# Kernel optimization log

Measured on AMD Instinct MI355X. Metric: run time of the kernel, lower is better.

Reference implementation:

```python
import jax, jax.numpy as jnp
import numpy as np

WS = 8   # window_size
SS = 4   # shift_size
NH = 6   # num_heads
EPS = 1e-5


def _win_partition(x, ws):
    # x: [B, H, W, C] -> [B * H/ws * W/ws, ws*ws, C]
    B, H, W, C = x.shape
    x = x.reshape(B, H // ws, ws, W // ws, ws, C)
    return x.transpose(0, 1, 3, 2, 4, 5).reshape(-1, ws * ws, C)


def _win_reverse(wins, ws, H, W, B):
    C = wins.shape[-1]
    x = wins.reshape(B, H // ws, W // ws, ws, ws, C)
    return x.transpose(0, 1, 3, 2, 4, 5).reshape(B, H, W, C)


def _rel_pos_index(ws):
    # static numpy computation, identical to the torch buffer
    coords = np.stack(np.meshgrid(np.arange(ws), np.arange(ws), indexing='ij')).reshape(2, -1)
    rel = coords[:, :, None] - coords[:, None, :]          # [2, N, N]
    rel = rel.transpose(1, 2, 0).copy()                    # [N, N, 2]
    rel[..., 0] += ws - 1
    rel[..., 1] += ws - 1
    rel[..., 0] *= 2 * ws - 1
    return rel.sum(-1)                                     # [N, N] int


def _attn_mask_np(H, W, ws, ss):
    # static numpy computation of the SW-MSA mask, identical to _compute_mask
    img = np.zeros((1, H, W, 1), np.float32)
    cnt = 0
    for hs in (slice(0, -ws), slice(-ws, -ss), slice(-ss, None)):
        for wsl in (slice(0, -ws), slice(-ws, -ss), slice(-ss, None)):
            img[:, hs, wsl, :] = cnt
            cnt += 1
    mw = img.reshape(1, H // ws, ws, W // ws, ws, 1).transpose(0, 1, 3, 2, 4, 5).reshape(-1, ws * ws)
    am = mw[:, None, :] - mw[:, :, None]                   # [nW, N, N]
    return np.where(am != 0, np.float32(-100.0), np.float32(0.0))


def _swin_forward(x, qkv_w, qkv_b, proj_w, proj_b, rpb_table,
                  norm2_g, norm2_b, mlp_w1, mlp_b1, mlp_w2, mlp_b2, H, W):
    B, L, C = x.shape
    ws, ss, nh = WS, SS, NH
    hd = C // nh
    x2d = x.reshape(B, H, W, C)
    shifted = jnp.roll(x2d, (-ss, -ss), axis=(1, 2))
    win = _win_partition(shifted, ws)                      # [B_, N, C]
    B_, N, _ = win.shape

    # --- window attention (note: original applies attention to un-normalized x) ---
    qkv = (win @ qkv_w + qkv_b).reshape(B_, N, 3, nh, hd)
    q = qkv[:, :, 0].transpose(0, 2, 1, 3)                 # [B_, nh, N, hd]
    k = qkv[:, :, 1].transpose(0, 2, 1, 3)
    v = qkv[:, :, 2].transpose(0, 2, 1, 3)
    attn = jnp.einsum('bhnd,bhmd->bhnm', q, k) * (hd ** -0.5)

    bias = rpb_table[jnp.asarray(_rel_pos_index(ws)).reshape(-1)]
    bias = bias.reshape(N, N, nh).transpose(2, 0, 1)       # [nh, N, N]
    attn = attn + bias[None]

    mask = jnp.asarray(_attn_mask_np(H, W, ws, ss))        # [nW, N, N]
    nW = mask.shape[0]
    attn = attn.reshape(B_ // nW, nW, nh, N, N) + mask[None, :, None]
    attn = jax.nn.softmax(attn.reshape(B_, nh, N, N), axis=-1)

    out = jnp.einsum('bhnm,bhmd->bnhd', attn, v).reshape(B_, N, C)
    out = out @ proj_w + proj_b

    x2d = _win_reverse(out, ws, H, W, B)
    x2d = jnp.roll(x2d, (ss, ss), axis=(1, 2))
    x = x + x2d.reshape(B, L, C)

    # --- MLP branch with LayerNorm (norm2) ---
    mu = x.mean(-1, keepdims=True)
    var = x.var(-1, keepdims=True)
    xn = (x - mu) * jax.lax.rsqrt(var + EPS) * norm2_g + norm2_b
    h = jax.nn.gelu(xn @ mlp_w1 + mlp_b1, approximate=False)
    return x + (h @ mlp_w2 + mlp_b2)


def setup_inputs() -> dict:
    B, H, W, C = 8, 128, 128, 192
    mlp_hidden = 4 * C
    ks = jax.random.split(jax.random.key(0), 6)
    std = 0.02
    return {
        'x': jax.random.normal(ks[0], (B, H * W, C), jnp.float32),
        'qkv_w': jax.random.normal(ks[1], (C, 3 * C), jnp.float32) * std,
        'qkv_b': jnp.zeros((3 * C,), jnp.float32),
        'proj_w': jax.random.normal(ks[2], (C, C), jnp.float32) * std,
        'proj_b': jnp.zeros((C,), jnp.float32),
        'rpb_table': jax.random.normal(ks[3], ((2 * WS - 1) ** 2, NH), jnp.float32) * std,
        'norm2_g': jnp.ones((C,), jnp.float32),
        'norm2_b': jnp.zeros((C,), jnp.float32),
        'mlp_w1': jax.random.normal(ks[4], (C, mlp_hidden), jnp.float32) * std,
        'mlp_b1': jnp.zeros((mlp_hidden,), jnp.float32),
        'mlp_w2': jax.random.normal(ks[5], (mlp_hidden, C), jnp.float32) * std,
        'mlp_b2': jnp.zeros((C,), jnp.float32),
        'H': H,
        'W': W,
    }


def reference(x, qkv_w, qkv_b, proj_w, proj_b, rpb_table, norm2_g, norm2_b,
              mlp_w1, mlp_b1, mlp_w2, mlp_b2, H, W):
    return _swin_forward(x, qkv_w, qkv_b, proj_w, proj_b, rpb_table,
                         norm2_g, norm2_b, mlp_w1, mlp_b1, mlp_w2, mlp_b2, H, W)
```

## Files before the change

kernel.cpp:

```cpp
#include <hip/hip_runtime.h>
#include <hip/hip_bf16.h>


typedef __hip_bfloat16 bf16;
typedef __attribute__((ext_vector_type(8))) short bfrag;
typedef __attribute__((ext_vector_type(4))) float ffrag;

__device__ __forceinline__ float b2f(bf16 v) { return __bfloat162float(v); }
__device__ __forceinline__ bf16  f2b(float v) { return __float2bfloat16(v); }

#define MFMA(a, b, c) __builtin_amdgcn_mfma_f32_16x16x32_bf16((a), (b), (c), 0, 0, 0)

#define WS_XRES  0ULL
#define WS_QKVT  100663296ULL
#define WS_PROJT (WS_QKVT  + 230400ULL)
#define WS_W1T   (WS_PROJT + 76800ULL)
#define WS_W2T   (WS_W1T   + 307200ULL)
#define WS_SB    (WS_W2T   + 331776ULL)

__device__ __forceinline__ float gelu_t(float x) {
    float y = x * (1.5957691216057308f + 0.07135481627f * x * x);
    return x * (1.f / (1.f + __expf(-y)));
}

__global__ __launch_bounds__(256) void k_prep(
    const float* __restrict__ qkv_w, const float* __restrict__ proj_w,
    const float* __restrict__ w1, const float* __restrict__ w2,
    const float* __restrict__ rpb, char* __restrict__ ws)
{
    int i = blockIdx.x * 256 + threadIdx.x;
    bf16* qkvT  = (bf16*)(ws + WS_QKVT);
    bf16* projT = (bf16*)(ws + WS_PROJT);
    bf16* w1T   = (bf16*)(ws + WS_W1T);
    bf16* w2T   = (bf16*)(ws + WS_W2T);
    bf16* sbB   = (bf16*)(ws + WS_SB);

    if (i < 115200) {
        int c = i / 200, k = i % 200;
        qkvT[i] = f2b(k < 192 ? qkv_w[k * 576 + c] : 0.f);
    } else if (i < 153600) {
        int j = i - 115200;
        int c = j / 200, k = j % 200;
        projT[j] = f2b(k < 192 ? proj_w[k * 192 + c] : 0.f);
    } else if (i < 307200) {
        int j = i - 153600;
        int c = j / 200, k = j % 200;
        w1T[j] = f2b(k < 192 ? w1[k * 768 + c] : 0.f);
    } else if (i < 473088) {
        int j = i - 307200;
        int kc = j / 13824, r = (j % 13824) / 72, kk = j % 72;
        w2T[j] = f2b(kk < 64 ? w2[(kc * 64 + kk) * 192 + r] : 0.f);
    } else {
        int j = i - 473088;
        int cls = j / 24576, h = (j % 24576) / 4096;
        int ii = (j % 4096) / 64, jj = j % 64;
        int ri = ii >> 3, ci = ii & 7, rj = jj >> 3, cj = jj & 7;
        float bias = rpb[(((ri - rj + 7) * 15) + (ci - cj + 7)) * 6 + h];
        int clsR = cls >> 1, clsC = cls & 1;
        int regi = (clsR ? (ri < 4 ? 1 : 2) : 0) * 3 + (clsC ? (ci < 4 ? 1 : 2) : 0);
        int regj = (clsR ? (rj < 4 ? 1 : 2) : 0) * 3 + (clsC ? (cj < 4 ? 1 : 2) : 0);
        sbB[j] = f2b(bias + (regi == regj ? 0.f : -100.f));
    }
}

__global__ __launch_bounds__(256, 2) void k_attn(
    const float* __restrict__ x, const float* __restrict__ qkv_b,
    const float* __restrict__ proj_b, const char* __restrict__ ws,
    float* __restrict__ xres)
{
    __shared__ __align__(16) unsigned char smem[75264];
    bf16* sXO = (bf16*)(smem);
    bf16* sQ  = (bf16*)(smem + 25600);
    bf16* sK  = (bf16*)(smem + 38912);
    bf16* sVT = (bf16*)(smem + 52224);
    bf16* sP  = (bf16*)(smem + 66048);

    const bf16* qkvT  = (const bf16*)(ws + WS_QKVT);
    const bf16* projT = (const bf16*)(ws + WS_PROJT);
    const bf16* sbB   = (const bf16*)(ws + WS_SB);

    const int t    = threadIdx.x;
    const int lane = t & 63, quad = lane >> 4, l15 = lane & 15;
    const int wave = t >> 6, r0 = wave * 16;
    const int win = blockIdx.x;
    const int b   = win >> 8;
    const int wi  = win & 255;
    const int wh  = wi >> 4, wwi = wi & 15;

    {
        int row = t >> 2;
        int cg  = (t & 3) * 48;
        int r = row >> 3, c = row & 7;
        int hs  = (wh * 8 + r + 4) & 127;
        int wsX = (wwi * 8 + c + 4) & 127;
        const float4* src = (const float4*)(x + ((size_t)(b * 16384 + hs * 128 + wsX)) * 192 + cg);
        __hip_bfloat162* dst = (__hip_bfloat162*)&sXO[row * 200 + cg];
        #pragma unroll
        for (int u = 0; u < 12; u++) {
            float4 f = src[u];
            dst[u * 2]     = __float22bfloat162_rn({f.x, f.y});
            dst[u * 2 + 1] = __float22bfloat162_rn({f.z, f.w});
        }
    }
    __syncthreads();

    bfrag aX[6];
    #pragma unroll
    for (int kb = 0; kb < 6; kb++)
        aX[kb] = *(const bfrag*)&sXO[(r0 + l15) * 200 + kb * 32 + quad * 8];

    const int cls = ((wh == 15) ? 2 : 0) + ((wwi == 15) ? 1 : 0);
    const bf16* bBc = sbB + (size_t)cls * 24576;

    bf16* sPw = sP + wave * 16 * 72;

    for (int g = 0; g < 2; g++) {
        if (g) __syncthreads();
        #pragma unroll
        for (int part = 0; part < 3; part++) {
            #pragma unroll
            for (int ct = 0; ct < 6; ct++) {
                int col = part * 192 + g * 96 + ct * 16 + l15;
                bfrag bw[6];
                #pragma unroll
                for (int kb = 0; kb < 6; kb++)
                    bw[kb] = *(const bfrag*)&qkvT[col * 200 + kb * 32 + quad * 8];
                ffrag acc = {0.f, 0.f, 0.f, 0.f};
                #pragma unroll
                for (int kb = 0; kb < 6; kb++) acc = MFMA(aX[kb], bw[kb], acc);
                float bias = qkv_b[col];
                #pragma unroll
                for (int reg = 0; reg < 4; reg++) {
                    int r = r0 + quad * 4 + reg;
                    float v = acc[reg] + bias;
                    if (part == 0)      sQ[r * 104 + ct * 16 + l15] = f2b(v);
                    else if (part == 1) sK[r * 104 + ct * 16 + l15] = f2b(v);
                    else {
                        int c96 = ct * 16 + l15;
                        sVT[((c96 >> 5) * 32 + (c96 & 31)) * 72 + r] = f2b(v);
                    }
                }
            }
        }
        __syncthreads();
        for (int hl = 0; hl < 3; hl++) {
            int h = g * 3 + hl;
            bfrag aQ = *(const bfrag*)&sQ[(r0 + l15) * 104 + hl * 32 + quad * 8];
            ffrag Sf[4];
            #pragma unroll
            for (int jt = 0; jt < 4; jt++) {
                bfrag bK = *(const bfrag*)&sK[(jt * 16 + l15) * 104 + hl * 32 + quad * 8];
                ffrag z = {0.f, 0.f, 0.f, 0.f};
                Sf[jt] = MFMA(aQ, bK, z);
            }
            const bf16* bb = bBc + h * 4096 + (r0 + quad * 4) * 64 + l15;
            #pragma unroll
            for (int jt = 0; jt < 4; jt++)
                #pragma unroll
                for (int reg = 0; reg < 4; reg++)
                    Sf[jt][reg] = Sf[jt][reg] * 0.1767766952966369f
                                + b2f(bb[reg * 64 + jt * 16]);
            #pragma unroll
            for (int reg = 0; reg < 4; reg++) {
                float m = fmaxf(fmaxf(Sf[0][reg], Sf[1][reg]), fmaxf(Sf[2][reg], Sf[3][reg]));
                m = fmaxf(m, __shfl_xor(m, 1)); m = fmaxf(m, __shfl_xor(m, 2));
                m = fmaxf(m, __shfl_xor(m, 4)); m = fmaxf(m, __shfl_xor(m, 8));
                float s = 0.f;
                #pragma unroll
                for (int jt = 0; jt < 4; jt++) { Sf[jt][reg] = __expf(Sf[jt][reg] - m); s += Sf[jt][reg]; }
                s += __shfl_xor(s, 1); s += __shfl_xor(s, 2);
                s += __shfl_xor(s, 4); s += __shfl_xor(s, 8);
                float inv = 1.f / s;
                int prow = (quad * 4 + reg) * 72;
                #pragma unroll
                for (int jt = 0; jt < 4; jt++)
                    sPw[prow + jt * 16 + l15] = f2b(Sf[jt][reg] * inv);
            }
            bfrag aP0 = *(const bfrag*)&sPw[l15 * 72 + quad * 8];
            bfrag aP1 = *(const bfrag*)&sPw[l15 * 72 + 32 + quad * 8];
            #pragma unroll
            for (int ct = 0; ct < 2; ct++) {
                bfrag bV0 = *(const bfrag*)&sVT[(hl * 32 + ct * 16 + l15) * 72 + quad * 8];
                bfrag bV1 = *(const bfrag*)&sVT[(hl * 32 + ct * 16 + l15) * 72 + 32 + quad * 8];
                ffrag z = {0.f, 0.f, 0.f, 0.f};
                ffrag o = MFMA(aP1, bV1, MFMA(aP0, bV0, z));
                #pragma unroll
                for (int reg = 0; reg < 4; reg++)
                    sXO[(r0 + quad * 4 + reg) * 200 + h * 32 + ct * 16 + l15] = f2b(o[reg]);
            }
        }
    }

    bfrag aO[6];
    #pragma unroll
    for (int kb = 0; kb < 6; kb++)
        aO[kb] = *(const bfrag*)&sXO[(r0 + l15) * 200 + kb * 32 + quad * 8];

    size_t tokb[4];
    #pragma unroll
    for (int reg = 0; reg < 4; reg++) {
        int n = r0 + quad * 4 + reg;
        int sr = wh * 8 + (n >> 3), scc = wwi * 8 + (n & 7);
        int h2 = (sr + 4) & 127, w2c = (scc + 4) & 127;
        tokb[reg] = ((size_t)(b * 16384 + h2 * 128 + w2c)) * 192;
    }

    #pragma unroll
    for (int ct = 0; ct < 12; ct++) {
        int col = ct * 16 + l15;
        bfrag bw[6];
        #pragma unroll
        for (int kb = 0; kb < 6; kb++)
            bw[kb] = *(const bfrag*)&projT[col * 200 + kb * 32 + quad * 8];
        ffrag acc = {0.f, 0.f, 0.f, 0.f};
        #pragma unroll
        for (int kb = 0; kb < 6; kb++) acc = MFMA(aO[kb], bw[kb], acc);
        float pb = proj_b[col];
        #pragma unroll
        for (int reg = 0; reg < 4; reg++)
            xres[tokb[reg] + col] = acc[reg] + pb + x[tokb[reg] + col];
    }
}

__global__ __launch_bounds__(256, 2) void k_mlp(
    const float* __restrict__ xres, const float* __restrict__ g,
    const float* __restrict__ bb, const float* __restrict__ b1,
    const float* __restrict__ b2, const char* __restrict__ ws,
    float* __restrict__ out)
{
    __shared__ __align__(16) unsigned char smem[69632];
    bf16* xnS = (bf16*)(smem);
    bf16* hS  = (bf16*)(smem + 51200);

    const bf16* w1T = (const bf16*)(ws + WS_W1T);
    const bf16* w2T = (const bf16*)(ws + WS_W2T);

    const int t    = threadIdx.x;
    const int lane = t & 63, quad = lane >> 4, l15 = lane & 15;
    const int wave = t >> 6, r0 = wave * 32;
    const size_t row0 = (size_t)blockIdx.x * 128;

    #pragma unroll
    for (int p = 0; p < 2; p++) {
        int row = r0 + p * 16 + l15;
        const float4* src = (const float4*)(xres + (row0 + row) * 192 + quad * 48);
        float v[48];
        float s = 0.f, sq = 0.f;
        #pragma unroll
        for (int u = 0; u < 12; u++) {
            float4 f = src[u];
            v[u*4] = f.x; v[u*4+1] = f.y; v[u*4+2] = f.z; v[u*4+3] = f.w;
            s  += f.x + f.y + f.z + f.w;
            sq += f.x*f.x + f.y*f.y + f.z*f.z + f.w*f.w;
        }
        s  += __shfl_xor(s, 16);  s  += __shfl_xor(s, 32);
        sq += __shfl_xor(sq, 16); sq += __shfl_xor(sq, 32);
        float mean = s * (1.f / 192.f);
        float var  = sq * (1.f / 192.f) - mean * mean;
        float rstd = rsqrtf(var + 1e-5f);
        __hip_bfloat162* dst = (__hip_bfloat162*)&xnS[row * 200 + quad * 48];
        #pragma unroll
        for (int u = 0; u < 24; u++) {
            int c = quad * 48 + u * 2;
            float a0 = (v[u*2]   - mean) * rstd * g[c]     + bb[c];
            float a1 = (v[u*2+1] - mean) * rstd * g[c + 1] + bb[c + 1];
            dst[u] = __float22bfloat162_rn({a0, a1});
        }
    }

    bfrag aX[2][6];
    #pragma unroll
    for (int rt = 0; rt < 2; rt++)
        #pragma unroll
        for (int kb = 0; kb < 6; kb++)
            aX[rt][kb] = *(const bfrag*)&xnS[(r0 + rt*16 + l15) * 200 + kb*32 + quad*8];

    ffrag oacc[2][12];
    #pragma unroll
    for (int rt = 0; rt < 2; rt++)
        #pragma unroll
        for (int ct = 0; ct < 12; ct++)
            oacc[rt][ct] = (ffrag){0.f, 0.f, 0.f, 0.f};

    for (int kc = 0; kc < 12; kc++) {
        #pragma unroll
        for (int ct = 0; ct < 4; ct++) {
            int col = kc * 64 + ct * 16 + l15;
            bfrag bw[6];
            #pragma unroll
            for (int kb = 0; kb < 6; kb++)
                bw[kb] = *(const bfrag*)&w1T[col * 200 + kb * 32 + quad * 8];
            float bias = b1[col];
            #pragma unroll
            for (int rt = 0; rt < 2; rt++) {
                ffrag a = {0.f, 0.f, 0.f, 0.f};
                #pragma unroll
                for (int kb = 0; kb < 6; kb++) a = MFMA(aX[rt][kb], bw[kb], a);
                #pragma unroll
                for (int reg = 0; reg < 4; reg++)
                    hS[(r0 + rt*16 + quad*4 + reg) * 72 + ct*16 + l15] =
                        f2b(gelu_t(a[reg] + bias));
            }
        }
        bfrag aH[2][2];
        #pragma unroll
        for (int rt = 0; rt < 2; rt++)
            #pragma unroll
            for (int k0 = 0; k0 < 2; k0++)
                aH[rt][k0] = *(const bfrag*)&hS[(r0 + rt*16 + l15) * 72 + k0*32 + quad*8];
        #pragma unroll
        for (int ct = 0; ct < 12; ct++) {
            bfrag bw2[2];
            #pragma unroll
            for (int k0 = 0; k0 < 2; k0++)
                bw2[k0] = *(const bfrag*)&w2T[(kc*192 + ct*16 + l15) * 72 + k0*32 + quad*8];
            #pragma unroll
            for (int rt = 0; rt < 2; rt++)
                #pragma unroll
                for (int k0 = 0; k0 < 2; k0++)
                    oacc[rt][ct] = MFMA(aH[rt][k0], bw2[k0], oacc[rt][ct]);
        }
    }

    #pragma unroll
    for (int rt = 0; rt < 2; rt++)
        #pragma unroll
        for (int ct = 0; ct < 12; ct++) {
            int col = ct * 16 + l15;
            float b2v = b2[col];
            #pragma unroll
            for (int reg = 0; reg < 4; reg++) {
                size_t gi = (row0 + r0 + rt*16 + quad*4 + reg) * 192 + col;
                out[gi] = xres[gi] + oacc[rt][ct][reg] + b2v;
            }
        }
}

extern "C" void kernel_launch(void* const* d_in, const int* in_sizes, int n_in,
                              void* d_out, int out_size, void* d_ws, size_t ws_size,
                              hipStream_t stream)
{
    (void)in_sizes; (void)n_in; (void)out_size; (void)ws_size;

    const float* x      = (const float*)d_in[0];
    const float* qkv_w  = (const float*)d_in[1];
    const float* qkv_b  = (const float*)d_in[2];
    const float* proj_w = (const float*)d_in[3];
    const float* proj_b = (const float*)d_in[4];
    const float* rpb    = (const float*)d_in[5];
    const float* n2g    = (const float*)d_in[6];
    const float* n2b    = (const float*)d_in[7];
    const float* w1     = (const float*)d_in[8];
    const float* b1     = (const float*)d_in[9];
    const float* w2     = (const float*)d_in[10];
    const float* b2     = (const float*)d_in[11];

    char*  ws   = (char*)d_ws;
    float* xres = (float*)(ws + WS_XRES);
    float* out  = (float*)d_out;

    hipLaunchKernelGGL(k_prep, dim3(2232), dim3(256), 0, stream,
                       qkv_w, proj_w, w1, w2, rpb, ws);
    hipLaunchKernelGGL(k_attn, dim3(2048), dim3(256), 0, stream,
                       x, qkv_b, proj_b, ws, xres);
    hipLaunchKernelGGL(k_mlp,  dim3(1024), dim3(256), 0, stream,
                       xres, n2g, n2b, b1, b2, ws, out);
}
```

Baseline: 566.9 us.

## Stage weight tiles into LDS via direct global-to-LDS loads and split projection kernel

Weights for the QKV, projection and MLP GEMMs are now copied into shared memory with global_load_lds in chunks, instead of each wave reading B-fragments straight from global memory. The output projection moves into a separate k_proj kernel that handles 128 rows per block, which lets it reuse the staged weights. The attention output makes an extra round trip through global memory as bf16 to feed that kernel. QKV weights are regrouped per head group and padded, and input rows are loaded straight into registers, skipping the LDS pass. In exchange this adds a kernel launch, extra global traffic for the intermediate, and more barriers.

```diff
diff --git a/kernel.cpp b/kernel.cpp
--- a/kernel.cpp
+++ b/kernel.cpp
@@ -6,17 +6,33 @@
 typedef __attribute__((ext_vector_type(8))) short bfrag;
 typedef __attribute__((ext_vector_type(4))) float ffrag;
 
+union bfu { bf16 h[8]; bfrag v; };
+
 __device__ __forceinline__ float b2f(bf16 v) { return __bfloat162float(v); }
 __device__ __forceinline__ bf16  f2b(float v) { return __float2bfloat16(v); }
 
 #define MFMA(a, b, c) __builtin_amdgcn_mfma_f32_16x16x32_bf16((a), (b), (c), 0, 0, 0)
 
 #define WS_XRES  0ULL
-#define WS_QKVT  100663296ULL
-#define WS_PROJT (WS_QKVT  + 230400ULL)
-#define WS_W1T   (WS_PROJT + 76800ULL)
-#define WS_W2T   (WS_W1T   + 307200ULL)
-#define WS_SB    (WS_W2T   + 331776ULL)
+#define WS_OG    100663296ULL
+#define WS_QKVTG 150994944ULL
+#define WS_QBG   151250944ULL
+#define WS_PROJT 151253504ULL
+#define WS_W1T   151330304ULL
+#define WS_W2T   151637504ULL
+#define WS_SB    151969280ULL
+
+__device__ __forceinline__ void stage_lds(const void* g, void* l, int nbytes, int t) {
+    const int lane16 = (t & 63) * 16;
+    for (int base = (t >> 6) * 1024; base < nbytes; base += 4096) {
+        if (base + lane16 < nbytes) {
+            __builtin_amdgcn_global_load_lds(
+                (const __attribute__((address_space(1))) void*)((const char*)g + base + lane16),
+                (__attribute__((address_space(3))) void*)((char*)l + base),
+                16, 0, 0);
+        }
+    }
+}
 
 __device__ __forceinline__ float gelu_t(float x) {
     float y = x * (1.5957691216057308f + 0.07135481627f * x * x);
@@ -24,34 +40,51 @@
 }
 
 __global__ __launch_bounds__(256) void k_prep(
-    const float* __restrict__ qkv_w, const float* __restrict__ proj_w,
-    const float* __restrict__ w1, const float* __restrict__ w2,
-    const float* __restrict__ rpb, char* __restrict__ ws)
+    const float* __restrict__ qkv_w, const float* __restrict__ qkv_b,
+    const float* __restrict__ proj_w, const float* __restrict__ w1,
+    const float* __restrict__ w2, const float* __restrict__ rpb,
+    char* __restrict__ ws)
 {
     int i = blockIdx.x * 256 + threadIdx.x;
-    bf16* qkvT  = (bf16*)(ws + WS_QKVT);
-    bf16* projT = (bf16*)(ws + WS_PROJT);
-    bf16* w1T   = (bf16*)(ws + WS_W1T);
-    bf16* w2T   = (bf16*)(ws + WS_W2T);
-    bf16* sbB   = (bf16*)(ws + WS_SB);
-
-    if (i < 115200) {
-        int c = i / 200, k = i % 200;
-        qkvT[i] = f2b(k < 192 ? qkv_w[k * 576 + c] : 0.f);
-    } else if (i < 153600) {
-        int j = i - 115200;
+    bf16*  qkvTg = (bf16*)(ws + WS_QKVTG);
+    float* qbg   = (float*)(ws + WS_QBG);
+    bf16*  projT = (bf16*)(ws + WS_PROJT);
+    bf16*  w1T   = (bf16*)(ws + WS_W1T);
+    bf16*  w2T   = (bf16*)(ws + WS_W2T);
+    bf16*  sbB   = (bf16*)(ws + WS_SB);
+
+    if (i < 128000) {
+        int g = i / 64000, rem = i % 64000;
+        int c = rem / 200, k = rem % 200;
+        float v = 0.f;
+        if (k < 192) {
+            if (c < 96)       v = qkv_w[k * 576 + g * 96 + c];
+            else if (c < 192) v = qkv_w[k * 576 + 192 + g * 96 + (c - 96)];
+            else if (c < 288) v = qkv_w[k * 576 + 384 + g * 96 + (c - 192)];
+        }
+        qkvTg[i] = f2b(v);
+    } else if (i < 128640) {
+        int j = i - 128000;
+        int g = j / 320, c = j % 320;
+        float v = 0.f;
+        if (c < 96)       v = qkv_b[g * 96 + c];
+        else if (c < 192) v = qkv_b[192 + g * 96 + (c - 96)];
+        else if (c < 288) v = qkv_b[384 + g * 96 + (c - 192)];
+        qbg[j] = v;
+    } else if (i < 167040) {
+        int j = i - 128640;
         int c = j / 200, k = j % 200;
         projT[j] = f2b(k < 192 ? proj_w[k * 192 + c] : 0.f);
-    } else if (i < 307200) {
-        int j = i - 153600;
+    } else if (i < 320640) {
+        int j = i - 167040;
         int c = j / 200, k = j % 200;
         w1T[j] = f2b(k < 192 ? w1[k * 768 + c] : 0.f);
-    } else if (i < 473088) {
-        int j = i - 307200;
+    } else if (i < 486528) {
+        int j = i - 320640;
         int kc = j / 13824, r = (j % 13824) / 72, kk = j % 72;
         w2T[j] = f2b(kk < 64 ? w2[(kc * 64 + kk) * 192 + r] : 0.f);
-    } else {
-        int j = i - 473088;
+    } else if (i < 584832) {
+        int j = i - 486528;
         int cls = j / 24576, h = (j % 24576) / 4096;
         int ii = (j % 4096) / 64, jj = j % 64;
         int ri = ii >> 3, ci = ii & 7, rj = jj >> 3, cj = jj & 7;
@@ -64,20 +97,19 @@
 }
 
 __global__ __launch_bounds__(256, 2) void k_attn(
-    const float* __restrict__ x, const float* __restrict__ qkv_b,
-    const float* __restrict__ proj_b, const char* __restrict__ ws,
-    float* __restrict__ xres)
+    const float* __restrict__ x, const char* __restrict__ ws,
+    bf16* __restrict__ Og)
 {
     __shared__ __align__(16) unsigned char smem[75264];
-    bf16* sXO = (bf16*)(smem);
+    bf16* sW  = (bf16*)(smem);
     bf16* sQ  = (bf16*)(smem + 25600);
     bf16* sK  = (bf16*)(smem + 38912);
     bf16* sVT = (bf16*)(smem + 52224);
     bf16* sP  = (bf16*)(smem + 66048);
 
-    const bf16* qkvT  = (const bf16*)(ws + WS_QKVT);
-    const bf16* projT = (const bf16*)(ws + WS_PROJT);
-    const bf16* sbB   = (const bf16*)(ws + WS_SB);
+    const bf16*  qkvTg = (const bf16*)(ws + WS_QKVTG);
+    const float* qbg   = (const float*)(ws + WS_QBG);
+    const bf16*  sbB   = (const bf16*)(ws + WS_SB);
 
     const int t    = threadIdx.x;
     const int lane = t & 63, quad = lane >> 4, l15 = lane & 15;
@@ -87,57 +119,52 @@
     const int wi  = win & 255;
     const int wh  = wi >> 4, wwi = wi & 15;
 
+    bfrag aX[6];
     {
-        int row = t >> 2;
-        int cg  = (t & 3) * 48;
-        int r = row >> 3, c = row & 7;
-        int hs  = (wh * 8 + r + 4) & 127;
-        int wsX = (wwi * 8 + c + 4) & 127;
-        const float4* src = (const float4*)(x + ((size_t)(b * 16384 + hs * 128 + wsX)) * 192 + cg);
-        __hip_bfloat162* dst = (__hip_bfloat162*)&sXO[row * 200 + cg];
-        #pragma unroll
-        for (int u = 0; u < 12; u++) {
-            float4 f = src[u];
-            dst[u * 2]     = __float22bfloat162_rn({f.x, f.y});
-            dst[u * 2 + 1] = __float22bfloat162_rn({f.z, f.w});
-        }
-    }
-    __syncthreads();
-
-    bfrag aX[6];
-    #pragma unroll
-    for (int kb = 0; kb < 6; kb++)
-        aX[kb] = *(const bfrag*)&sXO[(r0 + l15) * 200 + kb * 32 + quad * 8];
+        int row = r0 + l15;
+        int rr = row >> 3, cc = row & 7;
+        int hs  = (wh * 8 + rr + 4) & 127;
+        int wsx = (wwi * 8 + cc + 4) & 127;
+        const float* xrow = x + ((size_t)(b * 16384 + hs * 128 + wsx)) * 192;
+        #pragma unroll
+        for (int kb = 0; kb < 6; kb++) {
+            float4 f0 = *(const float4*)(xrow + kb * 32 + quad * 8);
+            float4 f1 = *(const float4*)(xrow + kb * 32 + quad * 8 + 4);
+            bfu u;
+            u.h[0] = f2b(f0.x); u.h[1] = f2b(f0.y); u.h[2] = f2b(f0.z); u.h[3] = f2b(f0.w);
+            u.h[4] = f2b(f1.x); u.h[5] = f2b(f1.y); u.h[6] = f2b(f1.z); u.h[7] = f2b(f1.w);
+            aX[kb] = u.v;
+        }
+    }
 
     const int cls = ((wh == 15) ? 2 : 0) + ((wwi == 15) ? 1 : 0);
     const bf16* bBc = sbB + (size_t)cls * 24576;
-
     bf16* sPw = sP + wave * 16 * 72;
 
     for (int g = 0; g < 2; g++) {
-        if (g) __syncthreads();
-        #pragma unroll
-        for (int part = 0; part < 3; part++) {
-            #pragma unroll
-            for (int ct = 0; ct < 6; ct++) {
-                int col = part * 192 + g * 96 + ct * 16 + l15;
-                bfrag bw[6];
-                #pragma unroll
-                for (int kb = 0; kb < 6; kb++)
-                    bw[kb] = *(const bfrag*)&qkvT[col * 200 + kb * 32 + quad * 8];
-                ffrag acc = {0.f, 0.f, 0.f, 0.f};
-                #pragma unroll
-                for (int kb = 0; kb < 6; kb++) acc = MFMA(aX[kb], bw[kb], acc);
-                float bias = qkv_b[col];
-                #pragma unroll
-                for (int reg = 0; reg < 4; reg++) {
-                    int r = r0 + quad * 4 + reg;
-                    float v = acc[reg] + bias;
-                    if (part == 0)      sQ[r * 104 + ct * 16 + l15] = f2b(v);
-                    else if (part == 1) sK[r * 104 + ct * 16 + l15] = f2b(v);
-                    else {
-                        int c96 = ct * 16 + l15;
-                        sVT[((c96 >> 5) * 32 + (c96 & 31)) * 72 + r] = f2b(v);
+        for (int ch = 0; ch < 5; ch++) {
+            __syncthreads();
+            stage_lds(qkvTg + (size_t)(g * 320 + ch * 64) * 200, sW, 25600, t);
+            __syncthreads();
+            #pragma unroll
+            for (int ct = 0; ct < 4; ct++) {
+                int c0 = ch * 64 + ct * 16;
+                if (c0 < 288) {
+                    bfrag bw[6];
+                    #pragma unroll
+                    for (int kb = 0; kb < 6; kb++)
+                        bw[kb] = *(const bfrag*)&sW[(ct * 16 + l15) * 200 + kb * 32 + quad * 8];
+                    ffrag acc = {0.f, 0.f, 0.f, 0.f};
+                    #pragma unroll
+                    for (int kb = 0; kb < 6; kb++) acc = MFMA(aX[kb], bw[kb], acc);
+                    float bias = qbg[g * 320 + c0 + l15];
+                    #pragma unroll
+                    for (int reg = 0; reg < 4; reg++) {
+                        int r = r0 + quad * 4 + reg;
+                        float v = acc[reg] + bias;
+                        if (c0 < 96)       sQ[r * 104 + c0 + l15] = f2b(v);
+                        else if (c0 < 192) sK[r * 104 + (c0 - 96) + l15] = f2b(v);
+                        else               sVT[(c0 - 192 + l15) * 72 + r] = f2b(v);
                     }
                 }
             }
@@ -186,40 +213,85 @@
                 ffrag o = MFMA(aP1, bV1, MFMA(aP0, bV0, z));
                 #pragma unroll
                 for (int reg = 0; reg < 4; reg++)
-                    sXO[(r0 + quad * 4 + reg) * 200 + h * 32 + ct * 16 + l15] = f2b(o[reg]);
-            }
-        }
-    }
-
-    bfrag aO[6];
-    #pragma unroll
-    for (int kb = 0; kb < 6; kb++)
-        aO[kb] = *(const bfrag*)&sXO[(r0 + l15) * 200 + kb * 32 + quad * 8];
-
-    size_t tokb[4];
-    #pragma unroll
-    for (int reg = 0; reg < 4; reg++) {
-        int n = r0 + quad * 4 + reg;
-        int sr = wh * 8 + (n >> 3), scc = wwi * 8 + (n & 7);
-        int h2 = (sr + 4) & 127, w2c = (scc + 4) & 127;
-        tokb[reg] = ((size_t)(b * 16384 + h2 * 128 + w2c)) * 192;
-    }
+                    Og[((size_t)win * 64 + r0 + quad * 4 + reg) * 192 + h * 32 + ct * 16 + l15]
+                        = f2b(o[reg]);
+            }
+        }
+    }
+}
+
+__global__ __launch_bounds__(256, 2) void k_proj(
+    const float* __restrict__ x, const float* __restrict__ proj_b,
+    const char* __restrict__ ws, float* __restrict__ xres)
+{
+    __shared__ __align__(16) bf16 sWp[192 * 200];
+
+    const bf16* projT = (const bf16*)(ws + WS_PROJT);
+    const bf16* Og    = (const bf16*)(ws + WS_OG);
+
+    const int t    = threadIdx.x;
+    const int lane = t & 63, quad = lane >> 4, l15 = lane & 15;
+    const int wave = t >> 6, r0 = wave * 32;
+    const size_t row0 = (size_t)blockIdx.x * 128;
+
+    stage_lds(projT, sWp, 76800, t);
+
+    bfrag aO[2][6];
+    #pragma unroll
+    for (int rt = 0; rt < 2; rt++)
+        #pragma unroll
+        for (int kb = 0; kb < 6; kb++)
+            aO[rt][kb] = *(const bfrag*)&Og[(row0 + r0 + rt * 16 + l15) * 192 + kb * 32 + quad * 8];
+
+    size_t tokb[2][4];
+    #pragma unroll
+    for (int rt = 0; rt < 2; rt++)
+        #pragma unroll
+        for (int reg = 0; reg < 4; reg++) {
+            int n = r0 + rt * 16 + quad * 4 + reg;
+            int w2 = (int)(blockIdx.x * 2) + (n >> 6);
+            int nl = n & 63;
+            int b = w2 >> 8, wi = w2 & 255;
+            int wh = wi >> 4, wwi = wi & 15;
+            int sr = wh * 8 + (nl >> 3), sc = wwi * 8 + (nl & 7);
+            int h2 = (sr + 4) & 127, w2c = (sc + 4) & 127;
+            tokb[rt][reg] = ((size_t)(b * 16384 + h2 * 128 + w2c)) * 192;
+        }
+
+    __syncthreads();
+
+    ffrag acc[2][12];
+    #pragma unroll
+    for (int rt = 0; rt < 2; rt++)
+        #pragma unroll
+        for (int ct = 0; ct < 12; ct++)
+            acc[rt][ct] = (ffrag){0.f, 0.f, 0.f, 0.f};
 
     #pragma unroll
     for (int ct = 0; ct < 12; ct++) {
-        int col = ct * 16 + l15;
         bfrag bw[6];
         #pragma unroll
         for (int kb = 0; kb < 6; kb++)
-            bw[kb] = *(const bfrag*)&projT[col * 200 + kb * 32 + quad * 8];
-        ffrag acc = {0.f, 0.f, 0.f, 0.f};
-        #pragma unroll
-        for (int kb = 0; kb < 6; kb++) acc = MFMA(aO[kb], bw[kb], acc);
-        float pb = proj_b[col];
-        #pragma unroll
-        for (int reg = 0; reg < 4; reg++)
-            xres[tokb[reg] + col] = acc[reg] + pb + x[tokb[reg] + col];
-    }
+            bw[kb] = *(const bfrag*)&sWp[(ct * 16 + l15) * 200 + kb * 32 + quad * 8];
+        #pragma unroll
+        for (int rt = 0; rt < 2; rt++)
+            #pragma unroll
+            for (int kb = 0; kb < 6; kb++)
+                acc[rt][ct] = MFMA(aO[rt][kb], bw[kb], acc[rt][ct]);
+    }
+
+    #pragma unroll
+    for (int rt = 0; rt < 2; rt++)
+        #pragma unroll
+        for (int ct = 0; ct < 12; ct++) {
+            int col = ct * 16 + l15;
+            float pb = proj_b[col];
+            #pragma unroll
+            for (int reg = 0; reg < 4; reg++) {
+                size_t gi = tokb[rt][reg] + col;
+                xres[gi] = acc[rt][ct][reg] + pb + x[gi];
+            }
+        }
 }
 
 __global__ __launch_bounds__(256, 2) void k_mlp(
@@ -228,9 +300,10 @@
     const float* __restrict__ b2, const char* __restrict__ ws,
     float* __restrict__ out)
 {
-    __shared__ __align__(16) unsigned char smem[69632];
-    bf16* xnS = (bf16*)(smem);
-    bf16* hS  = (bf16*)(smem + 51200);
+    __shared__ __align__(16) unsigned char smem[71680];
+    bf16* U   = (bf16*)(smem);
+    bf16* W2s = (bf16*)(smem + 25600);
+    bf16* hS  = (bf16*)(smem + 53248);
 
     const bf16* w1T = (const bf16*)(ws + WS_W1T);
     const bf16* w2T = (const bf16*)(ws + WS_W2T);
@@ -258,7 +331,7 @@
         float mean = s * (1.f / 192.f);
         float var  = sq * (1.f / 192.f) - mean * mean;
         float rstd = rsqrtf(var + 1e-5f);
-        __hip_bfloat162* dst = (__hip_bfloat162*)&xnS[row * 200 + quad * 48];
+        __hip_bfloat162* dst = (__hip_bfloat162*)&U[row * 200 + quad * 48];
         #pragma unroll
         for (int u = 0; u < 24; u++) {
             int c = quad * 48 + u * 2;
@@ -273,7 +346,11 @@
     for (int rt = 0; rt < 2; rt++)
         #pragma unroll
         for (int kb = 0; kb < 6; kb++)
-            aX[rt][kb] = *(const bfrag*)&xnS[(r0 + rt*16 + l15) * 200 + kb*32 + quad*8];
+            aX[rt][kb] = *(const bfrag*)&U[(r0 + rt*16 + l15) * 200 + kb*32 + quad*8];
+
+    __syncthreads();
+
+    bf16* hs_w = hS + wave * 32 * 72;
 
     ffrag oacc[2][12];
     #pragma unroll
@@ -283,14 +360,18 @@
             oacc[rt][ct] = (ffrag){0.f, 0.f, 0.f, 0.f};
 
     for (int kc = 0; kc < 12; kc++) {
+        __syncthreads();
+        stage_lds(w1T + (size_t)kc * 64 * 200, U, 25600, t);
+        stage_lds(w2T + (size_t)kc * 13824, W2s, 27648, t);
+        __syncthreads();
+
         #pragma unroll
         for (int ct = 0; ct < 4; ct++) {
-            int col = kc * 64 + ct * 16 + l15;
             bfrag bw[6];
             #pragma unroll
             for (int kb = 0; kb < 6; kb++)
-                bw[kb] = *(const bfrag*)&w1T[col * 200 + kb * 32 + quad * 8];
-            float bias = b1[col];
+                bw[kb] = *(const bfrag*)&U[(ct*16 + l15) * 200 + kb*32 + quad*8];
+            float bias = b1[kc * 64 + ct * 16 + l15];
             #pragma unroll
             for (int rt = 0; rt < 2; rt++) {
                 ffrag a = {0.f, 0.f, 0.f, 0.f};
@@ -298,7 +379,7 @@
                 for (int kb = 0; kb < 6; kb++) a = MFMA(aX[rt][kb], bw[kb], a);
                 #pragma unroll
                 for (int reg = 0; reg < 4; reg++)
-                    hS[(r0 + rt*16 + quad*4 + reg) * 72 + ct*16 + l15] =
+                    hs_w[(rt*16 + quad*4 + reg) * 72 + ct*16 + l15] =
                         f2b(gelu_t(a[reg] + bias));
             }
         }
@@ -307,13 +388,13 @@
         for (int rt = 0; rt < 2; rt++)
             #pragma unroll
             for (int k0 = 0; k0 < 2; k0++)
-                aH[rt][k0] = *(const bfrag*)&hS[(r0 + rt*16 + l15) * 72 + k0*32 + quad*8];
+                aH[rt][k0] = *(const bfrag*)&hs_w[(rt*16 + l15) * 72 + k0*32 + quad*8];
         #pragma unroll
         for (int ct = 0; ct < 12; ct++) {
             bfrag bw2[2];
             #pragma unroll
             for (int k0 = 0; k0 < 2; k0++)
-                bw2[k0] = *(const bfrag*)&w2T[(kc*192 + ct*16 + l15) * 72 + k0*32 + quad*8];
+                bw2[k0] = *(const bfrag*)&W2s[(ct*16 + l15) * 72 + k0*32 + quad*8];
             #pragma unroll
             for (int rt = 0; rt < 2; rt++)
                 #pragma unroll
@@ -357,12 +438,15 @@
 
     char*  ws   = (char*)d_ws;
     float* xres = (float*)(ws + WS_XRES);
+    bf16*  Og   = (bf16*)(ws + WS_OG);
     float* out  = (float*)d_out;
 
-    hipLaunchKernelGGL(k_prep, dim3(2232), dim3(256), 0, stream,
-                       qkv_w, proj_w, w1, w2, rpb, ws);
+    hipLaunchKernelGGL(k_prep, dim3(2285), dim3(256), 0, stream,
+                       qkv_w, qkv_b, proj_w, w1, w2, rpb, ws);
     hipLaunchKernelGGL(k_attn, dim3(2048), dim3(256), 0, stream,
-                       x, qkv_b, proj_b, ws, xres);
+                       x, ws, Og);
+    hipLaunchKernelGGL(k_proj, dim3(1024), dim3(256), 0, stream,
+                       x, proj_b, ws, xres);
     hipLaunchKernelGGL(k_mlp,  dim3(1024), dim3(256), 0, stream,
                        xres, n2g, n2b, b1, b2, ws, out);
 }
```

Result: faster. 469.8 us (-17.1%).
